# Kernel optimization log

Hardware: AMD Instinct MI355X
Metric: run time of the kernel (lower is better)

The kernel has to match this reference:

```python
import jax, jax.numpy as jnp
import numpy as np

B, P = 8, 1024
NUM_BINS = 11


def setup_inputs() -> dict:
    key = jax.random.key(0)
    x = jax.random.normal(key, (B, P, 6), dtype=jnp.float32)
    return {"x": x, "num_bins": NUM_BINS}


def reference(x, num_bins):
    Bv, Pv, _ = x.shape
    eps = 1e-6
    pos = x[..., 0:3]            # [B,P,3]
    ori = x[..., 3:6]            # [B,P,3]

    # axis 1 = i (source point), axis 2 = j (pair point)
    delta = pos[:, None, :, :] - pos[:, :, None, :]          # pj - pi: [B,P,P,3]
    ni = ori[:, :, None, :]                                   # [B,P,1,3]
    nj = ori[:, None, :, :]                                   # [B,1,P,3]

    dist = jnp.sqrt(jnp.sum(delta * delta, axis=-1))          # [B,P,P]

    ni_b = jnp.broadcast_to(ni, delta.shape)
    v = jnp.cross(delta, ni_b, axis=-1)
    v = v / (jnp.linalg.norm(v, axis=-1, keepdims=True) + eps)
    w = jnp.cross(ni_b, v, axis=-1)
    w = w / (jnp.linalg.norm(w, axis=-1, keepdims=True) + eps)

    alpha = jnp.sum(v * nj, axis=-1)                          # [B,P,P]
    phi = jnp.sum(ni * delta, axis=-1) / (dist + eps)         # [B,P,P]
    theta = jnp.arctan2(jnp.sum(w * nj, axis=-1),
                        jnp.sum(ni * nj, axis=-1)) / jnp.pi   # [B,P,P]

    def to_idx(a):
        # map [-1,1] -> bin index, truncation toward zero like torch .to(int64)
        idx = ((a + 1.0) * 0.5 * num_bins).astype(jnp.int32)
        return jnp.minimum(idx, num_bins - 1)

    fpfh_idx = (to_idx(alpha) * num_bins + to_idx(phi)) * num_bins + to_idx(theta)
    fpfh_idx = fpfh_idx.reshape(Bv, Pv * Pv)                  # [B, P*P]

    # exclude diagonal (i == j) pairs via zero weight, equivalent to the
    # eye-masked gather in the original (diagonal entries are finite)
    offdiag = (1.0 - jnp.eye(Pv, dtype=jnp.float32)).reshape(Pv * Pv)
    weights = jnp.broadcast_to(offdiag, (Bv, Pv * Pv))

    num_dim_feat = num_bins * num_bins * num_bins
    freq = jnp.zeros((Bv, num_dim_feat), dtype=jnp.float32)
    freq = freq.at[jnp.arange(Bv)[:, None], fpfh_idx].add(weights)
    freq = freq / (Pv * (Pv - 1))
    return freq
```

## Files before the change

### kernel.cpp

```cpp
#include <hip/hip_runtime.h>

#define P 1024
#define NB 11
#define NBINS 1331
#define BATCH 8
#define TI 8
#define NBLK (P / TI)

#define RFL(f) __uint_as_float(__builtin_amdgcn_readfirstlane(__float_as_uint(f)))

__global__ __launch_bounds__(256) void fpfh_main(const float* __restrict__ x,
                                                 int* __restrict__ part,
                                                 int npart) {
    __shared__ int shist[NBINS];

    const int t  = threadIdx.x;
    const int b  = blockIdx.y;
    const int i0 = blockIdx.x * TI;
    const float* xb = x + b * (P * 6);

    for (int z = t; z < NBINS; z += 256) shist[z] = 0;

    float PIX[TI], PIY[TI], PIZ[TI], NIX[TI], NIY[TI], NIZ[TI], NII[TI], SNI[TI];
    #pragma unroll
    for (int il = 0; il < TI; ++il) {
        const float* xi = xb + (i0 + il) * 6;
        PIX[il] = RFL(xi[0]); PIY[il] = RFL(xi[1]); PIZ[il] = RFL(xi[2]);
        NIX[il] = RFL(xi[3]); NIY[il] = RFL(xi[4]); NIZ[il] = RFL(xi[5]);
        float nii = fmaf(NIX[il], NIX[il], fmaf(NIY[il], NIY[il], NIZ[il] * NIZ[il]));
        NII[il] = RFL(nii);
        SNI[il] = RFL(__builtin_amdgcn_sqrtf(nii));
    }

    float pjx[4], pjy[4], pjz[4], njx[4], njy[4], njz[4];
    #pragma unroll
    for (int jt = 0; jt < 4; ++jt) {
        const float* xj = xb + (jt * 256 + t) * 6;
        pjx[jt] = xj[0]; pjy[jt] = xj[1]; pjz[jt] = xj[2];
        njx[jt] = xj[3]; njy[jt] = xj[4]; njz[jt] = xj[5];
    }

    __syncthreads();

    #pragma unroll
    for (int jt = 0; jt < 4; ++jt) {
        const int j = jt * 256 + t;

        #pragma unroll
        for (int il = 0; il < TI; ++il) {
            const float dx = pjx[jt] - PIX[il];
            const float dy = pjy[jt] - PIY[il];
            const float dz = pjz[jt] - PIZ[il];

            const float dd    = fmaf(dx, dx, fmaf(dy, dy, dz * dz));
            const float nid   = fmaf(NIX[il], dx, fmaf(NIY[il], dy, NIZ[il] * dz));
            const float nidnj = fmaf(NIX[il], njx[jt],
                                fmaf(NIY[il], njy[jt], NIZ[il] * njz[jt]));
            const float ddnj  = fmaf(dx, njx[jt], fmaf(dy, njy[jt], dz * njz[jt]));

            const float cvx = fmaf(dy, NIZ[il], -(dz * NIY[il]));
            const float cvy = fmaf(dz, NIX[il], -(dx * NIZ[il]));
            const float cvz = fmaf(dx, NIY[il], -(dy * NIX[il]));
            const float cvdnj = fmaf(cvx, njx[jt],
                                fmaf(cvy, njy[jt], cvz * njz[jt]));

            float cvv = fmaxf(fmaf(dd, NII[il], -(nid * nid)), 0.0f);
            const float rs    = __builtin_amdgcn_rsqf(cvv);
            const float alpha = cvdnj * rs;
            const float scv   = cvv * rs;

            const float phi = nid * __builtin_amdgcn_rsqf(dd);

            const float y_t = fmaf(NII[il], ddnj, -(nid * nidnj));
            const float x_t = (SNI[il] * nidnj) * scv;
            const float tq  = x_t * __builtin_amdgcn_rcpf(__builtin_fabsf(y_t));
            int kk = (tq <  3.40568625f) + (tq <  0.86650494f) + (tq < 0.14377830f)
                   + (tq < -0.45668469f) + (tq < -1.55603037f);
            const int ith = (y_t < 0.0f) ? 5 - kk : 5 + kk;

            int ia = min((int)fmaf(alpha, 5.5f, 5.5f), NB - 1);
            int ip = min((int)fmaf(phi,   5.5f, 5.5f), NB - 1);

            int bin = (ia * NB + ip) * NB + ith;
            if (bin < 0) bin += NBINS;
            if ((j != i0 + il) && ((unsigned)bin < (unsigned)NBINS))
                atomicAdd(&shist[bin], 1);
        }
    }
    __syncthreads();

    if (npart == NBLK) {
        int* slot = part + (b * NBLK + blockIdx.x) * NBINS;
        for (int z = t; z < NBINS; z += 256) slot[z] = shist[z];
    } else {
        int* slot = part + (b * npart + (blockIdx.x % npart)) * NBINS;
        for (int z = t; z < NBINS; z += 256) {
            int c = shist[z];
            if (c) atomicAdd(&slot[z], c);
        }
    }
}

__global__ __launch_bounds__(256) void fpfh_reduce(const int* __restrict__ part,
                                                   float* __restrict__ out,
                                                   int npart) {
    const int idx = blockIdx.x * 256 + threadIdx.x;
    if (idx >= BATCH * NBINS) return;
    const int b   = idx / NBINS;
    const int bin = idx - b * NBINS;
    const int* p  = part + b * npart * NBINS + bin;
    int s = 0;
    #pragma unroll 8
    for (int k = 0; k < npart; ++k) s += p[k * NBINS];
    out[idx] = (float)s * (1.0f / 1047552.0f);
}

extern "C" void kernel_launch(void* const* d_in, const int* in_sizes, int n_in,
                              void* d_out, int out_size, void* d_ws, size_t ws_size,
                              hipStream_t stream) {
    const float* x = (const float*)d_in[0];
    float* out = (float*)d_out;
    int* part  = (int*)d_ws;

    const size_t slot_bytes = (size_t)BATCH * NBINS * sizeof(int);
    const size_t full_need  = slot_bytes * NBLK;
    int npart;
    if (ws_size >= full_need) {
        npart = NBLK;
    } else {
        npart = (int)(ws_size / slot_bytes);
        if (npart < 1)   npart = 1;
        if (npart > NBLK) npart = NBLK;
        hipMemsetAsync(d_ws, 0, slot_bytes * npart, stream);
    }

    dim3 grid(NBLK, BATCH);
    fpfh_main<<<grid, 256, 0, stream>>>(x, part, npart);

    const int nOut = BATCH * NBINS;
    fpfh_reduce<<<(nOut + 255) / 256, 256, 0, stream>>>(part, out, npart);
}
```

Baseline: 28.91 us.

## Split j range across two blocks per i-tile and parallelize partial reduction

Each block now covers half of the j points for its 8-row i-tile, doubling the grid to 256x8 blocks so more CUs are occupied, and adds a launch-bounds occupancy hint. The reduce kernel now assigns four lanes per output bin, each summing a strided subset of partials, combined with shuffles, to shorten the serial loop over the doubled partial count. In exchange there are twice as many per-block histogram zeroing and write-outs, and the reduce reads twice as many partials.

Measured after the change: 38.21 us. +32.2%, slower.

```diff
diff --git a/kernel.cpp b/kernel.cpp
--- a/kernel.cpp
+++ b/kernel.cpp
@@ -5,18 +5,21 @@
 #define NBINS 1331
 #define BATCH 8
 #define TI 8
-#define NBLK (P / TI)
+#define NIT (P / TI)
+#define NBLKB (NIT * 2)
 
 #define RFL(f) __uint_as_float(__builtin_amdgcn_readfirstlane(__float_as_uint(f)))
 
-__global__ __launch_bounds__(256) void fpfh_main(const float* __restrict__ x,
-                                                 int* __restrict__ part,
-                                                 int npart) {
+__global__ __launch_bounds__(256, 8) void fpfh_main(const float* __restrict__ x,
+                                                    int* __restrict__ part,
+                                                    int npart) {
     __shared__ int shist[NBINS];
 
-    const int t  = threadIdx.x;
-    const int b  = blockIdx.y;
-    const int i0 = blockIdx.x * TI;
+    const int t     = threadIdx.x;
+    const int b     = blockIdx.y;
+    const int itile = blockIdx.x >> 1;
+    const int jhalf = blockIdx.x & 1;
+    const int i0    = itile * TI;
     const float* xb = x + b * (P * 6);
 
     for (int z = t; z < NBINS; z += 256) shist[z] = 0;
@@ -32,10 +35,10 @@
         SNI[il] = RFL(__builtin_amdgcn_sqrtf(nii));
     }
 
-    float pjx[4], pjy[4], pjz[4], njx[4], njy[4], njz[4];
+    float pjx[2], pjy[2], pjz[2], njx[2], njy[2], njz[2];
     #pragma unroll
-    for (int jt = 0; jt < 4; ++jt) {
-        const float* xj = xb + (jt * 256 + t) * 6;
+    for (int jt = 0; jt < 2; ++jt) {
+        const float* xj = xb + (jhalf * 512 + jt * 256 + t) * 6;
         pjx[jt] = xj[0]; pjy[jt] = xj[1]; pjz[jt] = xj[2];
         njx[jt] = xj[3]; njy[jt] = xj[4]; njz[jt] = xj[5];
     }
@@ -43,8 +46,8 @@
     __syncthreads();
 
     #pragma unroll
-    for (int jt = 0; jt < 4; ++jt) {
-        const int j = jt * 256 + t;
+    for (int jt = 0; jt < 2; ++jt) {
+        const int j = jhalf * 512 + jt * 256 + t;
 
         #pragma unroll
         for (int il = 0; il < TI; ++il) {
@@ -89,8 +92,8 @@
     }
     __syncthreads();
 
-    if (npart == NBLK) {
-        int* slot = part + (b * NBLK + blockIdx.x) * NBINS;
+    if (npart == NBLKB) {
+        int* slot = part + (b * NBLKB + blockIdx.x) * NBINS;
         for (int z = t; z < NBINS; z += 256) slot[z] = shist[z];
     } else {
         int* slot = part + (b * npart + (blockIdx.x % npart)) * NBINS;
@@ -104,15 +107,21 @@
 __global__ __launch_bounds__(256) void fpfh_reduce(const int* __restrict__ part,
                                                    float* __restrict__ out,
                                                    int npart) {
-    const int idx = blockIdx.x * 256 + threadIdx.x;
-    if (idx >= BATCH * NBINS) return;
-    const int b   = idx / NBINS;
-    const int bin = idx - b * NBINS;
-    const int* p  = part + b * npart * NBINS + bin;
+    const int tid = blockIdx.x * 256 + threadIdx.x;
+    const int o   = tid >> 2;
+    const int q   = tid & 3;
     int s = 0;
-    #pragma unroll 8
-    for (int k = 0; k < npart; ++k) s += p[k * NBINS];
-    out[idx] = (float)s * (1.0f / 1047552.0f);
+    if (o < BATCH * NBINS) {
+        const int b   = o / NBINS;
+        const int bin = o - b * NBINS;
+        const int* p  = part + (size_t)b * npart * NBINS + bin;
+        for (int k = q; k < npart; k += 4)
+            s += p[(size_t)k * NBINS];
+    }
+    s += __shfl_xor(s, 1);
+    s += __shfl_xor(s, 2);
+    if (q == 0 && o < BATCH * NBINS)
+        out[o] = (float)s * (1.0f / 1047552.0f);
 }
 
 extern "C" void kernel_launch(void* const* d_in, const int* in_sizes, int n_in,
@@ -123,20 +132,20 @@
     int* part  = (int*)d_ws;
 
     const size_t slot_bytes = (size_t)BATCH * NBINS * sizeof(int);
-    const size_t full_need  = slot_bytes * NBLK;
+    const size_t need_excl  = slot_bytes * NBLKB;
     int npart;
-    if (ws_size >= full_need) {
-        npart = NBLK;
+    if (ws_size >= need_excl) {
+        npart = NBLKB;
     } else {
         npart = (int)(ws_size / slot_bytes);
-        if (npart < 1)   npart = 1;
-        if (npart > NBLK) npart = NBLK;
+        if (npart < 1)     npart = 1;
+        if (npart > NIT)   npart = NIT;
         hipMemsetAsync(d_ws, 0, slot_bytes * npart, stream);
     }
 
-    dim3 grid(NBLK, BATCH);
+    dim3 grid(NBLKB, BATCH);
     fpfh_main<<<grid, 256, 0, stream>>>(x, part, npart);
 
-    const int nOut = BATCH * NBINS;
-    fpfh_reduce<<<(nOut + 255) / 256, 256, 0, stream>>>(part, out, npart);
+    const int nThreads = BATCH * NBINS * 4;
+    fpfh_reduce<<<(nThreads + 255) / 256, 256, 0, stream>>>(part, out, npart);
 }
```
